# Performance work log

Hardware: AMD Instinct MI355X
Metric: run time of the kernel (lower is better)

## Reference

```python
import jax, jax.numpy as jnp
import numpy as np

N = 50000        # atoms
E = 1600000      # edges (precomputed radius graph)
H = 128          # hidden_channels
F = 64           # num_filters
G = 50           # num_gaussians
L = 3            # num_interactions
NG = 256         # graphs in batch
MAXZ = 100       # atomic-number vocabulary
CUTOFF = 10.0


def ssp(x):
    # ShiftedSoftplus
    return jax.nn.softplus(x) - jnp.log(2.0).astype(x.dtype)


def setup_inputs() -> dict:
    key = jax.random.key(0)
    ks = jax.random.split(key, 20)
    s = 0.1
    inp = {
        "z": jax.random.randint(ks[0], (N,), 0, MAXZ),
        "pos": jax.random.uniform(ks[1], (N, 3), dtype=jnp.float32) * 5.0,
        "batch": jnp.sort(jax.random.randint(ks[2], (N,), 0, NG)),
        "edge_index": jax.random.randint(ks[3], (2, E), 0, N),
        "emb": jax.random.normal(ks[4], (MAXZ, H), dtype=jnp.float32),
        # interaction-block params, stacked over L layers
        "mw1": jax.random.normal(ks[5], (L, G, F), dtype=jnp.float32) * s,
        "mb1": jnp.zeros((L, F), dtype=jnp.float32),
        "mw2": jax.random.normal(ks[6], (L, F, F), dtype=jnp.float32) * s,
        "mb2": jnp.zeros((L, F), dtype=jnp.float32),
        "l1w": jax.random.normal(ks[7], (L, H, F), dtype=jnp.float32) * s,  # no bias
        "l2w": jax.random.normal(ks[8], (L, F, H), dtype=jnp.float32) * s,
        "l2b": jnp.zeros((L, H), dtype=jnp.float32),
        "lw": jax.random.normal(ks[9], (L, H, H), dtype=jnp.float32) * s,
        "lb": jnp.zeros((L, H), dtype=jnp.float32),
        # output MLP
        "ow1": jax.random.normal(ks[10], (H, H // 2), dtype=jnp.float32) * s,
        "ob1": jnp.zeros((H // 2,), dtype=jnp.float32),
        "ow2": jax.random.normal(ks[11], (H // 2, 1), dtype=jnp.float32) * s,
        "ob2": jnp.zeros((1,), dtype=jnp.float32),
    }
    return inp


def reference(z, pos, batch, edge_index, emb, mw1, mb1, mw2, mb2,
              l1w, l2w, l2b, lw, lb, ow1, ob1, ow2, ob2):
    src = edge_index[0]  # j (message source)
    dst = edge_index[1]  # i (message target)

    h = emb[z]                                   # [N,H]

    # edge distances + Gaussian smearing
    d = jnp.linalg.norm(pos[src] - pos[dst], axis=-1)          # [E]
    offset = jnp.linspace(0.0, CUTOFF, G, dtype=jnp.float32)   # [G]
    coeff = -0.5 / (offset[1] - offset[0]) ** 2
    edge_attr = jnp.exp(coeff * (d[:, None] - offset) ** 2)    # [E,G]

    # cosine cutoff
    C = 0.5 * (jnp.cos(d * jnp.pi / CUTOFF) + 1.0)             # [E]

    for i in range(L):
        # per-edge filter MLP
        W = ssp(edge_attr @ mw1[i] + mb1[i]) @ mw2[i] + mb2[i]  # [E,F]
        W = W * C[:, None]
        xj = (h @ l1w[i])[src]                                  # gather [E,F]
        msg = xj * W                                            # [E,F]
        agg = jax.ops.segment_sum(msg, dst, num_segments=N)     # [N,F]
        x = agg @ l2w[i] + l2b[i]                               # [N,H]
        x = ssp(x)
        x = x @ lw[i] + lb[i]
        h = h + x                                               # residual

    # output network + per-graph sum readout
    h = ssp(h @ ow1 + ob1)
    h = h @ ow2 + ob2                                           # [N,1]
    out = jax.ops.segment_sum(h, batch, num_segments=NG)        # [NG,1]
    return out.squeeze(1)                                       # [NG]
```

## Files before the change

### kernel.cpp

```cpp
#include <hip/hip_runtime.h>


typedef short bf16x8 __attribute__((ext_vector_type(8)));
typedef unsigned short ushort8 __attribute__((ext_vector_type(8)));
typedef float floatx4 __attribute__((ext_vector_type(4)));

#define HCH 128
#define FCH 64
#define GCH 50
#define LN  3
#define TBL 4096
#define CAP1 6144
#define CHUNK 1024
#define DMAX 8.6603f

#define MFMA(a, b, c) __builtin_amdgcn_mfma_f32_16x16x32_bf16((a), (b), (c), 0, 0, 0)

__device__ __forceinline__ unsigned short f2bf(float x) {
    unsigned int u = __float_as_uint(x);
    unsigned int r = (u + 0x7FFFu + ((u >> 16) & 1u)) >> 16;
    return (unsigned short)r;
}

__device__ __forceinline__ unsigned pk2bf(float lo, float hi) {
    unsigned ulo = __float_as_uint(lo) + 0x8000u;
    unsigned uhi = __float_as_uint(hi) + 0x8000u;
    return __builtin_amdgcn_perm(uhi, ulo, 0x07060302u);
}

__device__ __forceinline__ float bf2f(unsigned short u) {
    return __uint_as_float((unsigned)u << 16);
}

__device__ __forceinline__ float sspf(float x) {
    float t = __expf(-fabsf(x));
    float l = __logf(1.f + t);
    return fmaxf(x, 0.f) + l - 0.69314718056f;
}

__device__ __forceinline__ void fill_frag(const float* __restrict__ src,
                                          short* __restrict__ dst,
                                          int K, int F, int Ksrc,
                                          int tid, int nthr)
{
    int kc = K >> 5;
    int total = (F >> 4) * kc * 512;
    for (int i = tid; i < total; i += nthr) {
        int j = i & 7;
        int lane = (i >> 3) & 63;
        int rest = i >> 9;
        int kk = rest % kc;
        int nt = rest / kc;
        int k = kk * 32 + ((lane >> 4) << 3) + j;
        int f = nt * 16 + (lane & 15);
        float v = (k < Ksrc) ? src[k * F + f] : 0.f;
        dst[i] = (short)f2bf(v);
    }
}

__global__ void k_prep(const float* __restrict__ l1w, const float* __restrict__ l2w,
                       const float* __restrict__ lw,  const float* __restrict__ ow1,
                       short* __restrict__ l1wp, short* __restrict__ l2wp,
                       short* __restrict__ lwp,  short* __restrict__ ow1p)
{
    int tid = blockIdx.x * blockDim.x + threadIdx.x;
    int nthr = gridDim.x * blockDim.x;
    for (int l = 0; l < LN; l++) {
        fill_frag(l1w + l * HCH * FCH, l1wp + l * 8192, 128, 64, 128, tid, nthr);
        fill_frag(l2w + l * FCH * HCH, l2wp + l * 8192, 64, 128, 64, tid, nthr);
        fill_frag(lw  + l * HCH * HCH, lwp  + l * 16384, 128, 128, 128, tid, nthr);
    }
    fill_frag(ow1, ow1p, 128, 64, 128, tid, nthr);
}

__global__ __launch_bounds__(64) void k_wtab(
    const float* __restrict__ mw1, const float* __restrict__ mb1,
    const float* __restrict__ mw2, const float* __restrict__ mb2,
    unsigned short* __restrict__ Wtb)
{
    __shared__ float sh[64];
    int blk = blockIdx.x;
    int l = blk / TBL, k = blk - l * TBL;
    int f = threadIdx.x;
    float d = (float)k * (DMAX / (float)(TBL - 1));
    const float step = 10.f / 49.f;
    const float coeff = -0.5f / (step * step);

    float t1 = mb1[l * 64 + f];
    const float* w1 = mw1 + l * GCH * 64;
    for (int g = 0; g < GCH; g++) {
        float u = d - (float)g * step;
        t1 += __expf(coeff * u * u) * w1[g * 64 + f];
    }
    sh[f] = sspf(t1);
    float acc = mb2[l * 64 + f];
    const float* w2 = mw2 + l * 64 * 64;
    for (int g = 0; g < 64; g++) acc += sh[g] * w2[g * 64 + f];
    float C = 0.5f * (__cosf(d * 0.31415926535897932f) + 1.f);
    Wtb[(size_t)blk * 64 + f] = f2bf(acc * C);
}

__global__ __launch_bounds__(256, 2) void k_s1(
    const int* __restrict__ ei, const float* __restrict__ pos,
    int* __restrict__ gcur, int2* __restrict__ ebuf, int E, int nb1)
{
    __shared__ int hist[512];
    __shared__ int lstart[512];
    __shared__ int lcur[512];
    __shared__ int gbase[512];
    __shared__ int wsum[4];
    __shared__ int2 stage[CHUNK];

    int t = threadIdx.x, lane = t & 63, w = t >> 6;
    int e0 = blockIdx.x * CHUNK;
    int e1 = min(e0 + CHUNK, E);
    int cnt = e1 - e0;

    for (int i = t; i < 512; i += 256) hist[i] = 0;
    __syncthreads();

    int esrc[4], edst[4];
    float psx[4], psy[4], psz[4], pdx[4], pdy[4], pdz[4];
    bool val[4];
#pragma unroll
    for (int i = 0; i < 4; i++) {
        int e = e0 + t + i * 256;
        val[i] = e < e1;
        int ec = min(e, E - 1);
        esrc[i] = ei[ec];
        edst[i] = ei[E + ec];
    }
#pragma unroll
    for (int i = 0; i < 4; i++) {
        int s = esrc[i], d2 = edst[i];
        psx[i] = pos[s * 3 + 0]; psy[i] = pos[s * 3 + 1]; psz[i] = pos[s * 3 + 2];
        pdx[i] = pos[d2 * 3 + 0]; pdy[i] = pos[d2 * 3 + 1]; pdz[i] = pos[d2 * 3 + 2];
    }
    int2 my[4];
    int  mybk[4];
#pragma unroll
    for (int i = 0; i < 4; i++) {
        float dx = psx[i] - pdx[i];
        float dy = psy[i] - pdy[i];
        float dz = psz[i] - pdz[i];
        float dist = sqrtf(dx * dx + dy * dy + dz * dz);
        int tix = (int)(dist * ((float)(TBL - 1) / DMAX) + 0.5f);
        tix = (tix > TBL - 1) ? (TBL - 1) : tix;
        my[i] = make_int2(esrc[i] | (tix << 17), edst[i]);
        mybk[i] = val[i] ? (edst[i] >> 7) : -1;
        if (mybk[i] >= 0) atomicAdd(&hist[mybk[i]], 1);
    }
    __syncthreads();

    {
        int base = w * 128;
        int c0 = hist[base + lane];
        int c1 = hist[base + 64 + lane];
        int a = c0, b = c1;
#pragma unroll
        for (int o = 1; o < 64; o <<= 1) {
            int ua = __shfl_up(a, o, 64);
            int ub = __shfl_up(b, o, 64);
            if (lane >= o) { a += ua; b += ub; }
        }
        int atot = __shfl(a, 63, 64);
        b += atot;
        if (lane == 63) wsum[w] = b;
        __syncthreads();
        int prefix = 0;
#pragma unroll
        for (int i = 0; i < 4; i++) if (i < w) prefix += wsum[i];
        int ls0 = prefix + a - c0;
        int ls1 = prefix + b - c1;
        int bk0 = base + lane, bk1 = base + 64 + lane;
        lstart[bk0] = ls0; lcur[bk0] = ls0;
        lstart[bk1] = ls1; lcur[bk1] = ls1;
        int base0 = (c0 && bk0 < nb1) ? atomicAdd(&gcur[bk0 * 16], c0) : 0;
        int base1 = (c1 && bk1 < nb1) ? atomicAdd(&gcur[bk1 * 16], c1) : 0;
        gbase[bk0] = bk0 * CAP1 + base0;
        gbase[bk1] = bk1 * CAP1 + base1;
    }
    __syncthreads();

#pragma unroll
    for (int i = 0; i < 4; i++) {
        if (mybk[i] >= 0) {
            int ofs = atomicAdd(&lcur[mybk[i]], 1);
            stage[ofs] = my[i];
        }
    }
    __syncthreads();

    for (int i = t; i < cnt; i += 256) {
        int2 ed = stage[i];
        int bk = ed.y >> 7;
        int g = gbase[bk] + (i - lstart[bk]);
        if (g < bk * CAP1 + CAP1) ebuf[g] = ed;
    }
}

__global__ __launch_bounds__(512) void k_s2(
    const int2* __restrict__ ebuf, const int* __restrict__ gcur,
    int2* __restrict__ edata, int nb1)
{
    __shared__ int hist[128];
    __shared__ int bcur[128];
    __shared__ int wred[8];
    int t = threadIdx.x, lane = t & 63, w = t >> 6, bk = blockIdx.x;
    int cnt = min(gcur[bk * 16], CAP1);

    int v = (t < bk && t < nb1) ? min(gcur[t * 16], CAP1) : 0;
#pragma unroll
    for (int o = 32; o; o >>= 1) v += __shfl_down(v, o, 64);
    if (lane == 0) wred[w] = v;
    if (t < 128) hist[t] = 0;
    __syncthreads();
    int gs = 0;
#pragma unroll
    for (int i = 0; i < 8; i++) gs += wred[i];

    const int2* eb = ebuf + (size_t)bk * CAP1;
    for (int i = t; i < cnt; i += 512)
        atomicAdd(&hist[eb[i].y & 127], 1);
    __syncthreads();
    int myc = (t < 128) ? hist[t] : 0;
    for (int o = 1; o < 128; o <<= 1) {
        int u = (t < 128 && t >= o) ? hist[t - o] : 0;
        __syncthreads();
        if (t < 128) hist[t] += u;
        __syncthreads();
    }
    if (t < 128) bcur[t] = gs + hist[t] - myc;
    __syncthreads();
    for (int i = t; i < cnt; i += 512) {
        int2 ed = eb[i];
        int dl = ed.y & 127;
        int p = atomicAdd(&bcur[dl], 1);
        edata[p] = ed;
    }
}

__global__ __launch_bounds__(256) void k_node0(const int* __restrict__ z,
    const float* __restrict__ emb, const short* __restrict__ l1wp0,
    float* __restrict__ h, unsigned short* __restrict__ xjb,
    float* __restrict__ agg, int N)
{
    __shared__ __align__(16) short A3[8192];
    __shared__ int zL[64];
    int t = threadIdx.x, lane = t & 63, w = t >> 6;
    int n0 = blockIdx.x * 64;
    if (t < 64) { int n = n0 + t; zL[t] = (n < N) ? z[n] : 0; }
    __syncthreads();
    for (int i = t; i < 4096; i += 256) {
        int n = n0 + (i >> 6);
        if (n < N) agg[(size_t)n * FCH + (i & 63)] = 0.f;
    }
#pragma unroll
    for (int m = 0; m < 16; m++) {
        int ii = lane + 64 * m;
        int rloc = ii >> 6;
        int k0 = (ii & 63) * 2;
        int n = n0 + w * 16 + rloc;
        float2 v = make_float2(0.f, 0.f);
        if (n < N) {
            v = *(const float2*)(&emb[(size_t)zL[w * 16 + rloc] * HCH + k0]);
            *(float2*)(&h[(size_t)n * HCH + k0]) = v;
        }
        unsigned pk = pk2bf(v.x, v.y);
        int si = w * 2048 + (k0 >> 5) * 512 + (rloc + 16 * ((k0 >> 3) & 3)) * 8 + (k0 & 7);
        *(unsigned*)(&A3[si]) = pk;
    }
    int quad = lane >> 4, col = lane & 15;
    const bf16x8* B = (const bf16x8*)l1wp0;
    bf16x8 af[4];
#pragma unroll
    for (int kk = 0; kk < 4; kk++)
        af[kk] = *(const bf16x8*)(&A3[w * 2048 + kk * 512 + lane * 8]);
#pragma unroll
    for (int nt = 0; nt < 4; nt++) {
        floatx4 c = {0.f, 0.f, 0.f, 0.f};
#pragma unroll
        for (int kk = 0; kk < 4; kk++) c = MFMA(af[kk], B[(nt * 4 + kk) * 64 + lane], c);
        int f = nt * 16 + col;
#pragma unroll
        for (int reg = 0; reg < 4; reg++) {
            int n = n0 + w * 16 + quad * 4 + reg;
            if (n < N) xjb[(size_t)n * FCH + f] = f2bf(c[reg]);
        }
    }
}

__global__ __launch_bounds__(256) void k_edge(
    const int2* __restrict__ edata, const unsigned short* __restrict__ xjb,
    const unsigned short* __restrict__ Wt, float* __restrict__ agg, int E)
{
    __shared__ float M[64 * 68];
    __shared__ int tD[64];

    int t = threadIdx.x, lane = t & 63, w = t >> 6;
    int r  = w * 16 + (lane >> 2);
    int fq = lane & 3;
    int eg = blockIdx.x * 64 + r;

    int2 ed = make_int2(0, -1);
    if (eg < E) ed = edata[eg];
    int src = ed.x & 0x1FFFF;
    int tix = ((unsigned)ed.x) >> 17;
    if (fq == 0) tD[r] = ed.y;

    const ushort8* Wr = (const ushort8*)(Wt + ((size_t)tix << 6) + fq * 16);
    const ushort8* X  = (const ushort8*)(xjb + ((size_t)src << 6) + fq * 16);
    ushort8 w0 = Wr[0];
    ushort8 w1 = Wr[1];
    ushort8 xA = X[0];
    ushort8 xB = X[1];

    float* Mr = &M[r * 68 + fq * 16];
    float4 m;
    m.x = bf2f(w0[0]) * bf2f(xA[0]); m.y = bf2f(w0[1]) * bf2f(xA[1]);
    m.z = bf2f(w0[2]) * bf2f(xA[2]); m.w = bf2f(w0[3]) * bf2f(xA[3]);
    *(float4*)(Mr + 0) = m;
    m.x = bf2f(w0[4]) * bf2f(xA[4]); m.y = bf2f(w0[5]) * bf2f(xA[5]);
    m.z = bf2f(w0[6]) * bf2f(xA[6]); m.w = bf2f(w0[7]) * bf2f(xA[7]);
    *(float4*)(Mr + 4) = m;
    m.x = bf2f(w1[0]) * bf2f(xB[0]); m.y = bf2f(w1[1]) * bf2f(xB[1]);
    m.z = bf2f(w1[2]) * bf2f(xB[2]); m.w = bf2f(w1[3]) * bf2f(xB[3]);
    *(float4*)(Mr + 8) = m;
    m.x = bf2f(w1[4]) * bf2f(xB[4]); m.y = bf2f(w1[5]) * bf2f(xB[5]);
    m.z = bf2f(w1[6]) * bf2f(xB[6]); m.w = bf2f(w1[7]) * bf2f(xB[7]);
    *(float4*)(Mr + 12) = m;

    {
        int f = lane;
        int base = w * 16;
        float a = 0.f;
        int cur = tD[base];
#pragma unroll
        for (int i = 0; i < 16; i++) {
            int d2 = tD[base + i];
            if (d2 != cur) {
                if (cur >= 0) unsafeAtomicAdd(&agg[(size_t)cur * FCH + f], a);
                a = 0.f; cur = d2;
            }
            a += M[(base + i) * 68 + f];
        }
        if (cur >= 0) unsafeAtomicAdd(&agg[(size_t)cur * FCH + f], a);
    }
}

__global__ __launch_bounds__(256) void k_update(
    float* __restrict__ agg, const short* __restrict__ l2wp,
    const float* __restrict__ l2b, const short* __restrict__ lwp,
    const float* __restrict__ lb,  const short* __restrict__ l1wp_next,
    float* __restrict__ h, unsigned short* __restrict__ xjb, int layer, int N)
{
    __shared__ __align__(16) short AR[8192];
    int t = threadIdx.x, lane = t & 63, w = t >> 6;
    int n0 = blockIdx.x * 64;
    short* WR = &AR[w * 2048];
#pragma unroll
    for (int m = 0; m < 8; m++) {
        int ii = lane + 64 * m;
        int rloc = ii >> 5;
        int k0 = (ii & 31) * 2;
        int n = n0 + w * 16 + rloc;
        float2 v = make_float2(0.f, 0.f);
        if (n < N) v = *(const float2*)(&agg[(size_t)n * FCH + k0]);
        unsigned pk = pk2bf(v.x, v.y);
        int si = (k0 >> 5) * 512 + (rloc + 16 * ((k0 >> 3) & 3)) * 8 + (k0 & 7);
        *(unsigned*)(&WR[si]) = pk;
    }
#pragma unroll
    for (int i = 0; i < 16; i++) {
        int n = n0 + w * 16 + i;
        if (n < N) agg[(size_t)n * FCH + lane] = 0.f;
    }
    int quad = lane >> 4, col = lane & 15;
    const bf16x8* Bl2 = (const bf16x8*)(l2wp + layer * 8192);
    const bf16x8* Blw = (const bf16x8*)(lwp + layer * 16384);
    const bf16x8* Bl1 = (const bf16x8*)l1wp_next;

    bf16x8 a0 = *(const bf16x8*)(&WR[lane * 8]);
    bf16x8 a1 = *(const bf16x8*)(&WR[512 + lane * 8]);
#pragma unroll
    for (int nt = 0; nt < 8; nt++) {
        float bias = l2b[layer * HCH + nt * 16 + col];
        floatx4 c = {bias, bias, bias, bias};
        c = MFMA(a0, Bl2[(nt * 2 + 0) * 64 + lane], c);
        c = MFMA(a1, Bl2[(nt * 2 + 1) * 64 + lane], c);
        int f = nt * 16 + col;
        int si0 = (f >> 5) * 512 + (16 * ((f >> 3) & 3)) * 8 + (f & 7);
#pragma unroll
        for (int reg = 0; reg < 4; reg++)
            WR[si0 + (quad * 4 + reg) * 8] = (short)f2bf(sspf(c[reg]));
    }
    bf16x8 af[4];
#pragma unroll
    for (int kk = 0; kk < 4; kk++)
        af[kk] = *(const bf16x8*)(&WR[kk * 512 + lane * 8]);
#pragma unroll
    for (int nt = 0; nt < 8; nt++) {
        float bias = lb[layer * HCH + nt * 16 + col];
        floatx4 c = {bias, bias, bias, bias};
#pragma unroll
        for (int kk = 0; kk < 4; kk++) c = MFMA(af[kk], Blw[(nt * 4 + kk) * 64 + lane], c);
        int f = nt * 16 + col;
        int si0 = (f >> 5) * 512 + (16 * ((f >> 3) & 3)) * 8 + (f & 7);
#pragma unroll
        for (int reg = 0; reg < 4; reg++) {
            int n = n0 + w * 16 + quad * 4 + reg;
            float hv = 0.f;
            if (n < N) {
                hv = h[(size_t)n * HCH + f] + c[reg];
                h[(size_t)n * HCH + f] = hv;
            }
            WR[si0 + (quad * 4 + reg) * 8] = (short)f2bf(hv);
        }
    }
#pragma unroll
    for (int kk = 0; kk < 4; kk++)
        af[kk] = *(const bf16x8*)(&WR[kk * 512 + lane * 8]);
#pragma unroll
    for (int nt = 0; nt < 4; nt++) {
        floatx4 c = {0.f, 0.f, 0.f, 0.f};
#pragma unroll
        for (int kk = 0; kk < 4; kk++) c = MFMA(af[kk], Bl1[(nt * 4 + kk) * 64 + lane], c);
        int f = nt * 16 + col;
#pragma unroll
        for (int reg = 0; reg < 4; reg++) {
            int n = n0 + w * 16 + quad * 4 + reg;
            if (n < N) xjb[(size_t)n * FCH + f] = f2bf(c[reg]);
        }
    }
}

__global__ __launch_bounds__(256) void k_final(
    const float* __restrict__ agg, const short* __restrict__ l2wp,
    const float* __restrict__ l2b, const short* __restrict__ lwp,
    const float* __restrict__ lb,  const short* __restrict__ ow1p,
    const float* __restrict__ ob1, const float* __restrict__ ow2,
    const float* __restrict__ ob2, const int* __restrict__ batch,
    const float* __restrict__ h, float* __restrict__ out, int layer, int N)
{
    __shared__ __align__(16) short AR[8192];
    __shared__ float R[64 * 17];
    int t = threadIdx.x, lane = t & 63, w = t >> 6;
    int n0 = blockIdx.x * 64;
    short* WR = &AR[w * 2048];
#pragma unroll
    for (int m = 0; m < 8; m++) {
        int ii = lane + 64 * m;
        int rloc = ii >> 5;
        int k0 = (ii & 31) * 2;
        int n = n0 + w * 16 + rloc;
        float2 v = make_float2(0.f, 0.f);
        if (n < N) v = *(const float2*)(&agg[(size_t)n * FCH + k0]);
        unsigned pk = pk2bf(v.x, v.y);
        int si = (k0 >> 5) * 512 + (rloc + 16 * ((k0 >> 3) & 3)) * 8 + (k0 & 7);
        *(unsigned*)(&WR[si]) = pk;
    }
    int quad = lane >> 4, col = lane & 15;
    const bf16x8* Bl2 = (const bf16x8*)(l2wp + layer * 8192);
    const bf16x8* Blw = (const bf16x8*)(lwp + layer * 16384);
    const bf16x8* Bow = (const bf16x8*)ow1p;

    bf16x8 a0 = *(const bf16x8*)(&WR[lane * 8]);
    bf16x8 a1 = *(const bf16x8*)(&WR[512 + lane * 8]);
#pragma unroll
    for (int nt = 0; nt < 8; nt++) {
        float bias = l2b[layer * HCH + nt * 16 + col];
        floatx4 c = {bias, bias, bias, bias};
        c = MFMA(a0, Bl2[(nt * 2 + 0) * 64 + lane], c);
        c = MFMA(a1, Bl2[(nt * 2 + 1) * 64 + lane], c);
        int f = nt * 16 + col;
        int si0 = (f >> 5) * 512 + (16 * ((f >> 3) & 3)) * 8 + (f & 7);
#pragma unroll
        for (int reg = 0; reg < 4; reg++)
            WR[si0 + (quad * 4 + reg) * 8] = (short)f2bf(sspf(c[reg]));
    }
    bf16x8 af[4];
#pragma unroll
    for (int kk = 0; kk < 4; kk++)
        af[kk] = *(const bf16x8*)(&WR[kk * 512 + lane * 8]);
#pragma unroll
    for (int nt = 0; nt < 8; nt++) {
        float bias = lb[layer * HCH + nt * 16 + col];
        floatx4 c = {bias, bias, bias, bias};
#pragma unroll
        for (int kk = 0; kk < 4; kk++) c = MFMA(af[kk], Blw[(nt * 4 + kk) * 64 + lane], c);
        int f = nt * 16 + col;
        int si0 = (f >> 5) * 512 + (16 * ((f >> 3) & 3)) * 8 + (f & 7);
#pragma unroll
        for (int reg = 0; reg < 4; reg++) {
            int n = n0 + w * 16 + quad * 4 + reg;
            float hv = 0.f;
            if (n < N) hv = h[(size_t)n * HCH + f] + c[reg];
            WR[si0 + (quad * 4 + reg) * 8] = (short)f2bf(hv);
        }
    }
#pragma unroll
    for (int kk = 0; kk < 4; kk++)
        af[kk] = *(const bf16x8*)(&WR[kk * 512 + lane * 8]);
    float p[4] = {0.f, 0.f, 0.f, 0.f};
#pragma unroll
    for (int nt = 0; nt < 4; nt++) {
        float bias = ob1[nt * 16 + col];
        floatx4 c = {bias, bias, bias, bias};
#pragma unroll
        for (int kk = 0; kk < 4; kk++) c = MFMA(af[kk], Bow[(nt * 4 + kk) * 64 + lane], c);
        float w2 = ow2[nt * 16 + col];
#pragma unroll
        for (int reg = 0; reg < 4; reg++) p[reg] += sspf(c[reg]) * w2;
    }
#pragma unroll
    for (int reg = 0; reg < 4; reg++)
        R[(w * 16 + quad * 4 + reg) * 17 + col] = p[reg];
    __syncthreads();
    if (t < 64) {
        int n = n0 + t;
        float v = 0.f;
        int g = -1;
        if (n < N) {
            v = ob2[0];
#pragma unroll
            for (int c2 = 0; c2 < 16; c2++) v += R[t * 17 + c2];
            g = batch[n];
        }
#pragma unroll
        for (int off2 = 1; off2 < 64; off2 <<= 1) {
            float vv = __shfl_down(v, off2, 64);
            int gg = __shfl_down(g, off2, 64);
            if (lane + off2 < 64 && gg == g) v += vv;
        }
        int gp = __shfl_up(g, 1, 64);
        bool head = (lane == 0) || (g != gp);
        if (head && g >= 0) unsafeAtomicAdd(&out[g], v);
    }
}

extern "C" void kernel_launch(void* const* d_in, const int* in_sizes, int n_in,
                              void* d_out, int out_size, void* d_ws, size_t ws_size,
                              hipStream_t stream)
{
    const int*   z    = (const int*)d_in[0];
    const float* pos  = (const float*)d_in[1];
    const int*   batc = (const int*)d_in[2];
    const int*   ei   = (const int*)d_in[3];
    const float* emb  = (const float*)d_in[4];
    const float* mw1  = (const float*)d_in[5];
    const float* mb1  = (const float*)d_in[6];
    const float* mw2  = (const float*)d_in[7];
    const float* mb2  = (const float*)d_in[8];
    const float* l1w  = (const float*)d_in[9];
    const float* l2w  = (const float*)d_in[10];
    const float* l2b  = (const float*)d_in[11];
    const float* lw   = (const float*)d_in[12];
    const float* lb   = (const float*)d_in[13];
    const float* ow1  = (const float*)d_in[14];
    const float* ob1  = (const float*)d_in[15];
    const float* ow2  = (const float*)d_in[16];
    const float* ob2  = (const float*)d_in[17];
    float* out = (float*)d_out;

    int N = in_sizes[0];
    int E = in_sizes[3] / 2;
    int nb1 = (N + 127) >> 7;

    char* ws = (char*)d_ws;
    size_t off = 0;
    auto alloc = [&](size_t bytes) {
        void* p = ws + off;
        off = (off + bytes + 255) & ~(size_t)255;
        return p;
    };
    float* h      = (float*)alloc((size_t)N * HCH * 4);
    unsigned short* xjb = (unsigned short*)alloc((size_t)N * FCH * 2);
    float* agg    = (float*)alloc((size_t)N * FCH * 4);
    int2*  ebuf   = (int2*)alloc((size_t)nb1 * CAP1 * 8);
    int2*  edata  = (int2*)alloc((size_t)E * 8);
    unsigned short* Wtab = (unsigned short*)alloc((size_t)LN * TBL * 64 * 2);
    int*   gcur   = (int*)alloc((size_t)nb1 * 64);
    short* l1wp   = (short*)alloc(LN * 8192 * 2);
    short* l2wp   = (short*)alloc(LN * 8192 * 2);
    short* lwp    = (short*)alloc(LN * 16384 * 2);
    short* ow1p   = (short*)alloc(8192 * 2);

    int NB = (N + 63) / 64;
    int EB = (E + 63) / 64;
    int S1B = (E + CHUNK - 1) / CHUNK;

    k_prep<<<32, 256, 0, stream>>>(l1w, l2w, lw, ow1, l1wp, l2wp, lwp, ow1p);
    k_wtab<<<LN * TBL, 64, 0, stream>>>(mw1, mb1, mw2, mb2, Wtab);
    hipMemsetAsync(gcur, 0, (size_t)nb1 * 64, stream);
    k_s1<<<S1B, 256, 0, stream>>>(ei, pos, gcur, ebuf, E, nb1);
    k_s2<<<nb1, 512, 0, stream>>>(ebuf, gcur, edata, nb1);
    hipMemsetAsync(out, 0, (size_t)out_size * sizeof(float), stream);

    k_node0<<<NB, 256, 0, stream>>>(z, emb, l1wp, h, xjb, agg, N);
    for (int l = 0; l < LN; l++) {
        k_edge<<<EB, 256, 0, stream>>>(edata, xjb,
                                       Wtab + (size_t)l * TBL * 64, agg, E);
        if (l < LN - 1) {
            k_update<<<NB, 256, 0, stream>>>(agg, l2wp, l2b, lwp, lb,
                                             l1wp + (l + 1) * 8192, h, xjb, l, N);
        } else {
            k_final<<<NB, 256, 0, stream>>>(agg, l2wp, l2b, lwp, lb, ow1p,
                                            ob1, ow2, ob2, batc, h, out, l, N);
        }
    }
}
```

Before: 382.5 us.

## Replace two-pass bucketed edge sort with counting sort via global atomics

The edge reordering by destination is rebuilt as a counting sort. A per-node histogram is built with global atomics, a single-block exclusive scan turns it into offsets, and a scatter kernel uses atomic offsets to write packed edge records. This drops the intermediate bucket buffer and its fixed capacity cap, which could silently drop edges. In exchange it brings 1.6M scattered global atomics, a serial one-block scan over 50k entries, and edges that are no longer in a stable order within each destination.

```diff
diff --git a/kernel.cpp b/kernel.cpp
--- a/kernel.cpp
+++ b/kernel.cpp
@@ -10,8 +10,6 @@
 #define GCH 50
 #define LN  3
 #define TBL 4096
-#define CAP1 6144
-#define CHUNK 1024
 #define DMAX 8.6603f
 
 #define MFMA(a, b, c) __builtin_amdgcn_mfma_f32_16x16x32_bf16((a), (b), (c), 0, 0, 0)
@@ -100,143 +98,108 @@
     Wtb[(size_t)blk * 64 + f] = f2bf(acc * C);
 }
 
-__global__ __launch_bounds__(256, 2) void k_s1(
+__global__ __launch_bounds__(256) void k_count(
+    const int* __restrict__ ei, int* __restrict__ cnt, int E)
+{
+    int t4 = (blockIdx.x * 256 + threadIdx.x) * 4;
+    if (((E & 3) == 0) && t4 + 3 < E) {
+        int4 d = *(const int4*)(ei + E + t4);
+        atomicAdd(&cnt[d.x], 1);
+        atomicAdd(&cnt[d.y], 1);
+        atomicAdd(&cnt[d.z], 1);
+        atomicAdd(&cnt[d.w], 1);
+    } else {
+#pragma unroll
+        for (int i = 0; i < 4; i++)
+            if (t4 + i < E) atomicAdd(&cnt[ei[E + t4 + i]], 1);
+    }
+}
+
+__global__ __launch_bounds__(1024) void k_scan(int* __restrict__ cnt, int N)
+{
+    __shared__ int wsum[16];
+    __shared__ int carry;
+    int t = threadIdx.x, lane = t & 63, w = t >> 6;
+    if (t == 0) carry = 0;
+    int nchunk = (N + 4095) >> 12;
+    for (int c = 0; c < nchunk; c++) {
+        int i0 = (c << 12) + t * 4;
+        int4 v = make_int4(0, 0, 0, 0);
+        bool full = (i0 + 3 < N);
+        if (full) {
+            v = *(const int4*)(cnt + i0);
+        } else {
+            if (i0 + 0 < N) v.x = cnt[i0 + 0];
+            if (i0 + 1 < N) v.y = cnt[i0 + 1];
+            if (i0 + 2 < N) v.z = cnt[i0 + 2];
+        }
+        int s1 = v.x + v.y, s2 = s1 + v.z, tot = s2 + v.w;
+        int s = tot;
+#pragma unroll
+        for (int o = 1; o < 64; o <<= 1) {
+            int u = __shfl_up(s, o, 64);
+            if (lane >= o) s += u;
+        }
+        if (lane == 63) wsum[w] = s;
+        __syncthreads();
+        int wpre = 0;
+#pragma unroll
+        for (int k = 0; k < 16; k++) wpre += (k < w) ? wsum[k] : 0;
+        int excl = carry + wpre + (s - tot);
+        int4 o4;
+        o4.x = excl; o4.y = excl + v.x; o4.z = excl + s1; o4.w = excl + s2;
+        if (full) {
+            *(int4*)(cnt + i0) = o4;
+        } else {
+            if (i0 + 0 < N) cnt[i0 + 0] = o4.x;
+            if (i0 + 1 < N) cnt[i0 + 1] = o4.y;
+            if (i0 + 2 < N) cnt[i0 + 2] = o4.z;
+        }
+        __syncthreads();
+        if (t == 1023) carry += wpre + s;
+        __syncthreads();
+    }
+}
+
+__global__ __launch_bounds__(256) void k_scatter(
     const int* __restrict__ ei, const float* __restrict__ pos,
-    int* __restrict__ gcur, int2* __restrict__ ebuf, int E, int nb1)
-{
-    __shared__ int hist[512];
-    __shared__ int lstart[512];
-    __shared__ int lcur[512];
-    __shared__ int gbase[512];
-    __shared__ int wsum[4];
-    __shared__ int2 stage[CHUNK];
-
-    int t = threadIdx.x, lane = t & 63, w = t >> 6;
-    int e0 = blockIdx.x * CHUNK;
-    int e1 = min(e0 + CHUNK, E);
-    int cnt = e1 - e0;
-
-    for (int i = t; i < 512; i += 256) hist[i] = 0;
-    __syncthreads();
-
-    int esrc[4], edst[4];
+    int* __restrict__ ofs, int2* __restrict__ edata, int E)
+{
+    int t4 = (blockIdx.x * 256 + threadIdx.x) * 4;
+    if (t4 >= E) return;
+    int s_[4], d_[4];
+    if (((E & 3) == 0) && t4 + 3 < E) {
+        int4 a = *(const int4*)(ei + t4);
+        int4 b = *(const int4*)(ei + E + t4);
+        s_[0] = a.x; s_[1] = a.y; s_[2] = a.z; s_[3] = a.w;
+        d_[0] = b.x; d_[1] = b.y; d_[2] = b.z; d_[3] = b.w;
+    } else {
+#pragma unroll
+        for (int i = 0; i < 4; i++) {
+            int ec = min(t4 + i, E - 1);
+            s_[i] = ei[ec];
+            d_[i] = ei[E + ec];
+        }
+    }
     float psx[4], psy[4], psz[4], pdx[4], pdy[4], pdz[4];
-    bool val[4];
 #pragma unroll
     for (int i = 0; i < 4; i++) {
-        int e = e0 + t + i * 256;
-        val[i] = e < e1;
-        int ec = min(e, E - 1);
-        esrc[i] = ei[ec];
-        edst[i] = ei[E + ec];
-    }
-#pragma unroll
-    for (int i = 0; i < 4; i++) {
-        int s = esrc[i], d2 = edst[i];
+        int s = s_[i], d2 = d_[i];
         psx[i] = pos[s * 3 + 0]; psy[i] = pos[s * 3 + 1]; psz[i] = pos[s * 3 + 2];
         pdx[i] = pos[d2 * 3 + 0]; pdy[i] = pos[d2 * 3 + 1]; pdz[i] = pos[d2 * 3 + 2];
     }
-    int2 my[4];
-    int  mybk[4];
 #pragma unroll
     for (int i = 0; i < 4; i++) {
-        float dx = psx[i] - pdx[i];
-        float dy = psy[i] - pdy[i];
-        float dz = psz[i] - pdz[i];
-        float dist = sqrtf(dx * dx + dy * dy + dz * dz);
-        int tix = (int)(dist * ((float)(TBL - 1) / DMAX) + 0.5f);
-        tix = (tix > TBL - 1) ? (TBL - 1) : tix;
-        my[i] = make_int2(esrc[i] | (tix << 17), edst[i]);
-        mybk[i] = val[i] ? (edst[i] >> 7) : -1;
-        if (mybk[i] >= 0) atomicAdd(&hist[mybk[i]], 1);
-    }
-    __syncthreads();
-
-    {
-        int base = w * 128;
-        int c0 = hist[base + lane];
-        int c1 = hist[base + 64 + lane];
-        int a = c0, b = c1;
-#pragma unroll
-        for (int o = 1; o < 64; o <<= 1) {
-            int ua = __shfl_up(a, o, 64);
-            int ub = __shfl_up(b, o, 64);
-            if (lane >= o) { a += ua; b += ub; }
-        }
-        int atot = __shfl(a, 63, 64);
-        b += atot;
-        if (lane == 63) wsum[w] = b;
-        __syncthreads();
-        int prefix = 0;
-#pragma unroll
-        for (int i = 0; i < 4; i++) if (i < w) prefix += wsum[i];
-        int ls0 = prefix + a - c0;
-        int ls1 = prefix + b - c1;
-        int bk0 = base + lane, bk1 = base + 64 + lane;
-        lstart[bk0] = ls0; lcur[bk0] = ls0;
-        lstart[bk1] = ls1; lcur[bk1] = ls1;
-        int base0 = (c0 && bk0 < nb1) ? atomicAdd(&gcur[bk0 * 16], c0) : 0;
-        int base1 = (c1 && bk1 < nb1) ? atomicAdd(&gcur[bk1 * 16], c1) : 0;
-        gbase[bk0] = bk0 * CAP1 + base0;
-        gbase[bk1] = bk1 * CAP1 + base1;
-    }
-    __syncthreads();
-
-#pragma unroll
-    for (int i = 0; i < 4; i++) {
-        if (mybk[i] >= 0) {
-            int ofs = atomicAdd(&lcur[mybk[i]], 1);
-            stage[ofs] = my[i];
-        }
-    }
-    __syncthreads();
-
-    for (int i = t; i < cnt; i += 256) {
-        int2 ed = stage[i];
-        int bk = ed.y >> 7;
-        int g = gbase[bk] + (i - lstart[bk]);
-        if (g < bk * CAP1 + CAP1) ebuf[g] = ed;
-    }
-}
-
-__global__ __launch_bounds__(512) void k_s2(
-    const int2* __restrict__ ebuf, const int* __restrict__ gcur,
-    int2* __restrict__ edata, int nb1)
-{
-    __shared__ int hist[128];
-    __shared__ int bcur[128];
-    __shared__ int wred[8];
-    int t = threadIdx.x, lane = t & 63, w = t >> 6, bk = blockIdx.x;
-    int cnt = min(gcur[bk * 16], CAP1);
-
-    int v = (t < bk && t < nb1) ? min(gcur[t * 16], CAP1) : 0;
-#pragma unroll
-    for (int o = 32; o; o >>= 1) v += __shfl_down(v, o, 64);
-    if (lane == 0) wred[w] = v;
-    if (t < 128) hist[t] = 0;
-    __syncthreads();
-    int gs = 0;
-#pragma unroll
-    for (int i = 0; i < 8; i++) gs += wred[i];
-
-    const int2* eb = ebuf + (size_t)bk * CAP1;
-    for (int i = t; i < cnt; i += 512)
-        atomicAdd(&hist[eb[i].y & 127], 1);
-    __syncthreads();
-    int myc = (t < 128) ? hist[t] : 0;
-    for (int o = 1; o < 128; o <<= 1) {
-        int u = (t < 128 && t >= o) ? hist[t - o] : 0;
-        __syncthreads();
-        if (t < 128) hist[t] += u;
-        __syncthreads();
-    }
-    if (t < 128) bcur[t] = gs + hist[t] - myc;
-    __syncthreads();
-    for (int i = t; i < cnt; i += 512) {
-        int2 ed = eb[i];
-        int dl = ed.y & 127;
-        int p = atomicAdd(&bcur[dl], 1);
-        edata[p] = ed;
+        if (t4 + i < E) {
+            float dx = psx[i] - pdx[i];
+            float dy = psy[i] - pdy[i];
+            float dz = psz[i] - pdz[i];
+            float dist = sqrtf(dx * dx + dy * dy + dz * dz);
+            int tix = (int)(dist * ((float)(TBL - 1) / DMAX) + 0.5f);
+            tix = (tix > TBL - 1) ? (TBL - 1) : tix;
+            int p = atomicAdd(&ofs[d_[i]], 1);
+            edata[p] = make_int2(s_[i] | (tix << 17), d_[i]);
+        }
     }
 }
 
@@ -564,7 +527,6 @@
 
     int N = in_sizes[0];
     int E = in_sizes[3] / 2;
-    int nb1 = (N + 127) >> 7;
 
     char* ws = (char*)d_ws;
     size_t off = 0;
@@ -576,10 +538,9 @@
     float* h      = (float*)alloc((size_t)N * HCH * 4);
     unsigned short* xjb = (unsigned short*)alloc((size_t)N * FCH * 2);
     float* agg    = (float*)alloc((size_t)N * FCH * 4);
-    int2*  ebuf   = (int2*)alloc((size_t)nb1 * CAP1 * 8);
     int2*  edata  = (int2*)alloc((size_t)E * 8);
     unsigned short* Wtab = (unsigned short*)alloc((size_t)LN * TBL * 64 * 2);
-    int*   gcur   = (int*)alloc((size_t)nb1 * 64);
+    int*   ofs    = (int*)alloc((size_t)N * 4);
     short* l1wp   = (short*)alloc(LN * 8192 * 2);
     short* l2wp   = (short*)alloc(LN * 8192 * 2);
     short* lwp    = (short*)alloc(LN * 16384 * 2);
@@ -587,13 +548,14 @@
 
     int NB = (N + 63) / 64;
     int EB = (E + 63) / 64;
-    int S1B = (E + CHUNK - 1) / CHUNK;
-
+    int ECB = (E + 1023) / 1024;
+
+    hipMemsetAsync(ofs, 0, (size_t)N * 4, stream);
     k_prep<<<32, 256, 0, stream>>>(l1w, l2w, lw, ow1, l1wp, l2wp, lwp, ow1p);
     k_wtab<<<LN * TBL, 64, 0, stream>>>(mw1, mb1, mw2, mb2, Wtab);
-    hipMemsetAsync(gcur, 0, (size_t)nb1 * 64, stream);
-    k_s1<<<S1B, 256, 0, stream>>>(ei, pos, gcur, ebuf, E, nb1);
-    k_s2<<<nb1, 512, 0, stream>>>(ebuf, gcur, edata, nb1);
+    k_count<<<ECB, 256, 0, stream>>>(ei, ofs, E);
+    k_scan<<<1, 1024, 0, stream>>>(ofs, N);
+    k_scatter<<<ECB, 256, 0, stream>>>(ei, pos, ofs, edata, E);
     hipMemsetAsync(out, 0, (size_t)out_size * sizeof(float), stream);
 
     k_node0<<<NB, 256, 0, stream>>>(z, emb, l1wp, h, xjb, agg, N);
```

Measured after the change: 515.3 us. 1.35x slower.
